# Kernel optimization log

Measured on AMD Instinct MI355X. Metric: run time of the kernel, lower is better.

Reference implementation:

```python
import jax, jax.numpy as jnp
import numpy as np

B, T, W, MODES, NL = 64, 4096, 64, 32, 4
OUT_T = 4096

def _gelu(x):
    # torch.nn.GELU default = exact erf form
    return jax.nn.gelu(x, approximate=False)

def setup_inputs() -> dict:
    key = jax.random.key(0)
    ks = jax.random.split(key, 16)
    scale = 1.0 / (W * W)
    return {
        "x": jax.random.normal(ks[0], (B, T), jnp.float32),
        "lift_w": jax.random.normal(ks[1], (W, 1), jnp.float32) * (1.0 / np.sqrt(1.0)),
        "lift_b": jax.random.normal(ks[2], (W,), jnp.float32) * 0.02,
        "spec_wr": jax.random.normal(ks[3], (NL, W, W, MODES), jnp.float32) * scale,
        "spec_wi": jax.random.normal(ks[4], (NL, W, W, MODES), jnp.float32) * scale,
        "pw_w": jax.random.normal(ks[5], (NL, W, W), jnp.float32) * (1.0 / np.sqrt(W)),
        "pw_b": jax.random.normal(ks[6], (NL, W), jnp.float32) * 0.02,
        "proj1_w": jax.random.normal(ks[7], (W, W), jnp.float32) * (1.0 / np.sqrt(W)),
        "proj1_b": jax.random.normal(ks[8], (W,), jnp.float32) * 0.02,
        "proj2_w": jax.random.normal(ks[9], (1, W), jnp.float32) * (1.0 / np.sqrt(W)),
        "proj2_b": jax.random.normal(ks[10], (1,), jnp.float32) * 0.02,
        "tok_w": jax.random.normal(ks[11], (OUT_T, T), jnp.float32) * (1.0 / np.sqrt(T)),
        "tok_b": jax.random.normal(ks[12], (OUT_T,), jnp.float32) * 0.02,
    }

def reference(x, lift_w, lift_b, spec_wr, spec_wi, pw_w, pw_b,
              proj1_w, proj1_b, proj2_w, proj2_b, tok_w, tok_b):
    # lift: [B,T,1] @ [1,W] -> [B,T,W] -> permute to [B,W,T]
    h = (x[..., None] * lift_w[:, 0][None, None, :] + lift_b)  # [B,T,W]
    h = jnp.transpose(h, (0, 2, 1))  # [B,W,T]
    n_freq = T // 2 + 1
    for l in range(NL):
        xf = jnp.fft.rfft(h, axis=-1)  # [B,W,n_freq] complex64
        w = spec_wr[l] + 1j * spec_wi[l]  # [W,W,MODES]
        out_m = jnp.einsum('bim,iom->bom', xf[:, :, :MODES], w)
        out_ft = jnp.pad(out_m, ((0, 0), (0, 0), (0, n_freq - MODES)))
        spec = jnp.fft.irfft(out_ft, n=T, axis=-1)  # [B,W,T] float32
        pw = jnp.einsum('oi,bit->bot', pw_w[l], h) + pw_b[l][None, :, None]
        h = _gelu(spec + pw)
    h = jnp.transpose(h, (0, 2, 1))  # [B,T,W]
    h = _gelu(h @ proj1_w.T + proj1_b)
    h = (h @ proj2_w.T + proj2_b)[..., 0]  # [B,T]
    return h @ tok_w.T + tok_b  # [B,OUT_T]
```

## Files before the change

kernel.cpp:

```cpp
#include <hip/hip_runtime.h>
#include <math.h>
#include <stdint.h>

#define BB 64
#define TT 4096
#define WW 64
#define MODES 32
#define NLAYER 4
#define OUTT 4096
#define KSPLIT 8
#define KSPLIT_L 16

typedef uint32_t u32;
typedef __attribute__((ext_vector_type(8))) short bf16x8;
typedef __attribute__((ext_vector_type(16))) float f32x16;

#define OFF_HC   0
#define OFF_FTH  16777216
#define OFF_FTL  16908288
#define OFF_ITH  17039360
#define OFF_ITL  17170432
#define OFF_PWH  17301504
#define OFF_PWL  17309696
#define OFF_P1H  17317888
#define OFF_P1L  17319936
#define OFF_YH   17321984
#define OFF_YL   17453056
#define OFF_XFP  17584128
#define OFF_XFB  21778432
#define OFF_SC   22040576
#define OFF_PWLW 22302720
#define OFF_PWLB 22302784
#define OFF_XFXP 22302848
#define OFF_XFXT 22335616

__device__ __forceinline__ float gelu_exact(float x) {
    float ax = fabsf(x);
    float z  = ax * 0.70710678118654752f;
    float t  = __builtin_amdgcn_rcpf(fmaf(0.3275911f, z, 1.0f));
    float ex = __builtin_amdgcn_exp2f(z * z * -1.44269504088896341f);
    float p  = fmaf(fmaf(fmaf(fmaf(1.061405429f, t, -1.453152027f),
                              t, 1.421413741f), t, -0.284496736f), t, 0.254829592f);
    float er = 1.0f - p * t * ex;
    er = copysignf(er, x);
    return 0.5f * x * (1.0f + er);
}
__device__ __forceinline__ u32 bfrn(float f) {
    u32 u = __float_as_uint(f);
    return (u + 0x7fffu + ((u >> 16) & 1u)) >> 16;
}
__device__ __forceinline__ u32 packf(float f) {
    u32 h = bfrn(f);
    float r = f - __uint_as_float(h << 16);
    u32 l = bfrn(r);
    return h | (l << 16);
}
__device__ __forceinline__ void unpack8(const u32* w, bf16x8& hi, bf16x8& lo) {
    union { bf16x8 v; ushort u[8]; } H, L;
    #pragma unroll
    for (int i = 0; i < 8; ++i) { H.u[i] = (ushort)(w[i] & 0xffffu); L.u[i] = (ushort)(w[i] >> 16); }
    hi = H.v; lo = L.v;
}
__device__ __forceinline__ void cvt8(const float* f, bf16x8& hi, bf16x8& lo) {
    union { bf16x8 v; ushort u[8]; } H, L;
    #pragma unroll
    for (int i = 0; i < 8; ++i) {
        u32 h = bfrn(f[i]);
        H.u[i] = (ushort)h;
        L.u[i] = (ushort)bfrn(f[i] - __uint_as_float(h << 16));
    }
    hi = H.v; lo = L.v;
}

#define MM3(ah, al, bh, bl, acc)                                          \
    acc = __builtin_amdgcn_mfma_f32_32x32x16_bf16(ah, bh, acc, 0, 0, 0);  \
    acc = __builtin_amdgcn_mfma_f32_32x32x16_bf16(ah, bl, acc, 0, 0, 0);  \
    acc = __builtin_amdgcn_mfma_f32_32x32x16_bf16(al, bh, acc, 0, 0, 0);

#define ACC_ZERO(acc) { _Pragma("unroll") for (int _i = 0; _i < 16; ++_i) acc[_i] = 0.0f; }

__global__ __launch_bounds__(256) void build_tables_kernel(ushort* __restrict__ fth, ushort* __restrict__ ftl,
                                                           ushort* __restrict__ ith, ushort* __restrict__ itl) {
    const int idx = blockIdx.x * 256 + threadIdx.x;
    const float w0 = 6.28318530717958647692f / (float)TT;
    {
        int pos = idx & 7, l = (idx >> 3) & 63, half = (idx >> 9) & 1, ttile = idx >> 10;
        int j = half * 32 + (l & 31);
        int t = ttile * 16 + (l >> 5) * 8 + pos;
        int m = j & 31;
        float ang = (float)((m * t) & (TT - 1)) * w0;
        float s, c; sincosf(ang, &s, &c);
        u32 p = packf((j < 32) ? c : -s);
        fth[idx] = (ushort)(p & 0xffffu); ftl[idx] = (ushort)(p >> 16);
    }
    {
        int pos = idx & 7, l = (idx >> 3) & 63, kt = (idx >> 9) & 3, t32 = idx >> 11;
        int t = t32 * 32 + (l & 31);
        int j = kt * 16 + (l >> 5) * 8 + pos;
        int m = j & 31;
        float ang = (float)((m * t) & (TT - 1)) * w0;
        float s, c; sincosf(ang, &s, &c);
        float v;
        if (j == 0)       v = 1.0f / (float)TT;
        else if (j < 32)  v = (2.0f / (float)TT) * c;
        else if (j == 32) v = 0.0f;
        else              v = -(2.0f / (float)TT) * s;
        u32 p = packf(v);
        ith[idx] = (ushort)(p & 0xffffu); itl[idx] = (ushort)(p >> 16);
    }
}

__global__ __launch_bounds__(256) void wconv_kernel(const float* __restrict__ pww, const float* __restrict__ p1w,
                                                    const float* __restrict__ lw, const float* __restrict__ lb,
                                                    const float* __restrict__ pwb,
                                                    ushort* __restrict__ pwh, ushort* __restrict__ pwl,
                                                    ushort* __restrict__ p1h, ushort* __restrict__ p1l,
                                                    float* __restrict__ pwlw, float* __restrict__ pwlb) {
    int idx = blockIdx.x * 256 + threadIdx.x;
    if (idx < NLAYER * 4096) {
        int pos = idx & 7, l = (idx >> 3) & 63, kt = (idx >> 9) & 3, half = (idx >> 11) & 1, layer = idx >> 12;
        int o = half * 32 + (l & 31);
        int w = kt * 16 + (l >> 5) * 8 + pos;
        u32 p = packf(pww[layer * 4096 + o * 64 + w]);
        pwh[idx] = (ushort)(p & 0xffffu); pwl[idx] = (ushort)(p >> 16);
    } else if (idx < NLAYER * 4096 + 4096) {
        int k = idx - NLAYER * 4096;
        int pos = k & 7, l = (k >> 3) & 63, kt = (k >> 9) & 3, half = (k >> 11) & 1;
        int wp = half * 32 + (l & 31);
        int w = kt * 16 + (l >> 5) * 8 + pos;
        u32 p = packf(p1w[wp * 64 + w]);
        p1h[k] = (ushort)(p & 0xffffu); p1l[k] = (ushort)(p >> 16);
    } else if (idx < NLAYER * 4096 + 4096 + 64) {
        int o = idx - (NLAYER * 4096 + 4096);
        float aw = 0.f, ab = 0.f;
        for (int w = 0; w < 64; ++w) {
            float pv = pww[o * 64 + w];
            aw += pv * lw[w];
            ab += pv * lb[w];
        }
        pwlw[o] = aw;
        pwlb[o] = ab + pwb[o];
    }
}

__device__ __forceinline__ size_t yfm_idx(int b, int o, int j) {
    return ((((size_t)b * 2 + (o >> 5)) * 4 + (j >> 4)) * 64 + (o & 31) + 32 * ((j >> 3) & 1)) * 8 + (j & 7);
}

__global__ __launch_bounds__(256) void dftx_kernel(const float* __restrict__ x,
                                                   const ushort* __restrict__ fth,
                                                   const ushort* __restrict__ ftl,
                                                   float* __restrict__ xfxp) {
    const int kc = blockIdx.x;
    const int tid = threadIdx.x, l = tid & 63, q = tid >> 6;
    const int mt = q >> 1, nt = q & 1;
    const int bc = nt * 32 + (l & 31);
    const int kh = (l >> 5) * 8;
    f32x16 acc; ACC_ZERO(acc);
    for (int ks = 0; ks < 32; ++ks) {
        int k0 = kc * 512 + ks * 16 + kh;
        size_t fo = (((size_t)(kc * 32 + ks) * 2 + mt) * 64 + l) * 8;
        bf16x8 ah = *(const bf16x8*)(fth + fo);
        bf16x8 al = *(const bf16x8*)(ftl + fo);
        float fbuf[8];
        *(float4*)(fbuf)     = *(const float4*)(x + (size_t)bc * TT + k0);
        *(float4*)(fbuf + 4) = *(const float4*)(x + (size_t)bc * TT + k0 + 4);
        bf16x8 bh, bl; cvt8(fbuf, bh, bl);
        MM3(ah, al, bh, bl, acc);
    }
    #pragma unroll
    for (int r = 0; r < 16; ++r) {
        int j = mt * 32 + (r & 3) + 8 * (r >> 2) + 4 * (l >> 5);
        xfxp[(size_t)kc * 4096 + j * 64 + bc] = acc[r];
    }
}

__global__ __launch_bounds__(256) void xfx_reduce_kernel(const float* __restrict__ xfxp,
                                                         float* __restrict__ xfxT) {
    int idx = blockIdx.x * 256 + threadIdx.x;
    float v = 0.f;
    #pragma unroll
    for (int kc = 0; kc < KSPLIT; ++kc) v += xfxp[(size_t)kc * 4096 + idx];
    xfxT[idx] = v;
}

__global__ __launch_bounds__(256) void specmix0_kernel(const float* __restrict__ xfxT,
                                                       const float* __restrict__ lw,
                                                       const float* __restrict__ lb,
                                                       const float* __restrict__ wr,
                                                       const float* __restrict__ wi,
                                                       ushort* __restrict__ yh,
                                                       ushort* __restrict__ yl) {
    int tid = blockIdx.x * 256 + threadIdx.x;
    int m = tid & 31, o = (tid >> 5) & 63, b = tid >> 11;
    float xvr = xfxT[m * 64 + b];
    float xvi = xfxT[(32 + m) * 64 + b];
    float c0 = (m == 0) ? (float)TT : 0.0f;
    float yr = 0.f, yim = 0.f;
    #pragma unroll 4
    for (int i = 0; i < WW; ++i) {
        float xr = lw[i] * xvr + c0 * lb[i];
        float xi = lw[i] * xvi;
        float ar = wr[((size_t)(i * 64 + o)) * 32 + m];
        float ai = wi[((size_t)(i * 64 + o)) * 32 + m];
        yr  += xr * ar - xi * ai;
        yim += xr * ai + xi * ar;
    }
    u32 pr = packf(yr), pi = packf(yim);
    size_t i0 = yfm_idx(b, o, m), i1 = yfm_idx(b, o, 32 + m);
    yh[i0] = (ushort)(pr & 0xffffu); yl[i0] = (ushort)(pr >> 16);
    yh[i1] = (ushort)(pi & 0xffffu); yl[i1] = (ushort)(pi >> 16);
}

__global__ __launch_bounds__(256) void specmix_kernel(const float* __restrict__ xfb,
                                                      const float* __restrict__ wr,
                                                      const float* __restrict__ wi,
                                                      ushort* __restrict__ yh,
                                                      ushort* __restrict__ yl) {
    int tid = blockIdx.x * 256 + threadIdx.x;
    int m = tid & 31, o = (tid >> 5) & 63, b = tid >> 11;
    float yr = 0.f, yim = 0.f;
    #pragma unroll 4
    for (int i = 0; i < WW; ++i) {
        float xr = xfb[((size_t)(b * 64 + m)) * 64 + i];
        float xi = xfb[((size_t)(b * 64 + 32 + m)) * 64 + i];
        float ar = wr[((size_t)(i * 64 + o)) * 32 + m];
        float ai = wi[((size_t)(i * 64 + o)) * 32 + m];
        yr  += xr * ar - xi * ai;
        yim += xr * ai + xi * ar;
    }
    u32 pr = packf(yr), pi = packf(yim);
    size_t i0 = yfm_idx(b, o, m), i1 = yfm_idx(b, o, 32 + m);
    yh[i0] = (ushort)(pr & 0xffffu); yl[i0] = (ushort)(pr >> 16);
    yh[i1] = (ushort)(pi & 0xffffu); yl[i1] = (ushort)(pi >> 16);
}

__global__ __launch_bounds__(256) void xreduce_kernel(const float* __restrict__ xfp,
                                                      float* __restrict__ xfb) {
    int idx = blockIdx.x * 256 + threadIdx.x;
    float v = 0.f;
    #pragma unroll
    for (int kc = 0; kc < KSPLIT_L; ++kc) v += xfp[(size_t)kc * 262144 + idx];
    xfb[idx] = v;
}

template<int IS_L0>
__global__ __launch_bounds__(256) void layer_kernel(u32* __restrict__ hc,
                                                    const ushort* __restrict__ yh, const ushort* __restrict__ yl,
                                                    const ushort* __restrict__ ith, const ushort* __restrict__ itl,
                                                    const ushort* __restrict__ pwh, const ushort* __restrict__ pwl,
                                                    const float* __restrict__ pwb,
                                                    const float* __restrict__ x,
                                                    const float* __restrict__ pwlw, const float* __restrict__ pwlb,
                                                    const ushort* __restrict__ fth, const ushort* __restrict__ ftl,
                                                    float* __restrict__ xfp) {
    __shared__ u32 lht[2][64 * 68];
    const int kc = blockIdx.x, b = blockIdx.y;
    const int tid = threadIdx.x, l = tid & 63, q = tid >> 6;
    const int mt = q >> 1, nt = q & 1;
    const int ltc = nt * 32 + (l & 31);
    const int kh = (l >> 5) * 8;
    f32x16 aF; ACC_ZERO(aF);

    u32 pf[32];
    if (!IS_L0) {
        const int t32g0 = (kc * 256 >> 5) + nt;
        #pragma unroll
        for (int ks = 0; ks < 4; ++ks) {
            const u32* p = hc + (((size_t)b * 128 + t32g0) * 4 + ks) * 512 + l * 8;
            *(uint4*)(pf + ks * 8)     = *(const uint4*)(p);
            *(uint4*)(pf + ks * 8 + 4) = *(const uint4*)(p + 4);
        }
    }

    for (int tile = 0; tile < 4; ++tile) {
        const int tbase = kc * 256 + tile * 64;
        const int t32g = (tbase >> 5) + nt;
        u32* lbuf = lht[tile & 1];
        f32x16 acc; ACC_ZERO(acc);
        #pragma unroll
        for (int ks = 0; ks < 4; ++ks) {
            size_t yo = (((size_t)b * 2 + mt) * 4 + ks) * 512 + l * 8;
            size_t io = ((size_t)t32g * 4 + ks) * 512 + l * 8;
            bf16x8 ya = *(const bf16x8*)(yh + yo);
            bf16x8 yb = *(const bf16x8*)(yl + yo);
            bf16x8 bh = *(const bf16x8*)(ith + io);
            bf16x8 bl = *(const bf16x8*)(itl + io);
            MM3(ya, yb, bh, bl, acc);
        }
        float xv = 0.f;
        if (!IS_L0) {
            #pragma unroll
            for (int ks = 0; ks < 4; ++ks) {
                size_t po = ((size_t)mt * 4 + ks) * 512 + l * 8;
                bf16x8 pa = *(const bf16x8*)(pwh + po);
                bf16x8 pb = *(const bf16x8*)(pwl + po);
                bf16x8 bh, bl; unpack8(pf + ks * 8, bh, bl);
                MM3(pa, pb, bh, bl, acc);
            }
            if (tile < 3) {
                const int t32n = t32g + 2;
                #pragma unroll
                for (int ks = 0; ks < 4; ++ks) {
                    const u32* p = hc + (((size_t)b * 128 + t32n) * 4 + ks) * 512 + l * 8;
                    *(uint4*)(pf + ks * 8)     = *(const uint4*)(p);
                    *(uint4*)(pf + ks * 8 + 4) = *(const uint4*)(p + 4);
                }
            }
        } else {
            xv = x[(size_t)b * TT + tbase + ltc];
        }
        u32 ov[16];
        #pragma unroll
        for (int rq = 0; rq < 4; ++rq) {
            int ob = mt * 32 + 8 * rq + 4 * (l >> 5);
            #pragma unroll
            for (int i = 0; i < 4; ++i) {
                float v = acc[rq * 4 + i];
                if (IS_L0) v += pwlw[ob + i] * xv + pwlb[ob + i];
                else       v += pwb[ob + i];
                ov[rq * 4 + i] = packf(gelu_exact(v));
            }
        }
        #pragma unroll
        for (int rq = 0; rq < 4; ++rq) {
            int ob = mt * 32 + 8 * rq + 4 * (l >> 5);
            #pragma unroll
            for (int i = 0; i < 4; ++i) lbuf[(ob + i) * 68 + ltc] = ov[rq * 4 + i];
        }
        __syncthreads();
        #pragma unroll
        for (int rq = 0; rq < 4; ++rq) {
            size_t ho = (((size_t)b * 128 + t32g) * 4 + (mt * 2 + (rq >> 1))) * 512
                      + ((l & 31) + 32 * (rq & 1)) * 8 + 4 * (l >> 5);
            *(uint4*)(hc + ho) = *(uint4*)(ov + rq * 4);
        }
        #pragma unroll
        for (int ks = 0; ks < 4; ++ks) {
            int k0 = ks * 16 + kh;
            size_t fo = (((size_t)((tbase >> 4) + ks)) * 2 + mt) * 512 + l * 8;
            bf16x8 ah = *(const bf16x8*)(fth + fo);
            bf16x8 al = *(const bf16x8*)(ftl + fo);
            u32 wbuf[8];
            *(uint4*)(wbuf)     = *(const uint4*)&lbuf[ltc * 68 + k0];
            *(uint4*)(wbuf + 4) = *(const uint4*)&lbuf[ltc * 68 + k0 + 4];
            bf16x8 bh, bl; unpack8(wbuf, bh, bl);
            MM3(ah, al, bh, bl, aF);
        }
    }
    float* dst = xfp + ((size_t)(kc * 64 + b)) * 4096;
    #pragma unroll
    for (int r = 0; r < 16; ++r) {
        int j = mt * 32 + (r & 3) + 8 * (r >> 2) + 4 * (l >> 5);
        dst[j * 64 + ltc] = aF[r];
    }
}

__global__ __launch_bounds__(256) void layer3_kernel(const u32* __restrict__ hc,
                                                     const ushort* __restrict__ yh, const ushort* __restrict__ yl,
                                                     const ushort* __restrict__ ith, const ushort* __restrict__ itl,
                                                     const ushort* __restrict__ pwh, const ushort* __restrict__ pwl,
                                                     const float* __restrict__ pwb,
                                                     const ushort* __restrict__ p1h, const ushort* __restrict__ p1l,
                                                     const float* __restrict__ p1b,
                                                     const float* __restrict__ p2w, const float* __restrict__ p2b,
                                                     u32* __restrict__ sc) {
    __shared__ u32 lht[64 * 68];
    __shared__ float red[4][64];
    const int t0 = blockIdx.x << 6, b = blockIdx.y;
    const int tid = threadIdx.x, l = tid & 63, q = tid >> 6;
    const int mt = q >> 1, nt = q & 1;
    const int ltc = nt * 32 + (l & 31);
    const int kh = (l >> 5) * 8;
    const int t32g = (t0 >> 5) + nt;
    f32x16 acc; ACC_ZERO(acc);

    #pragma unroll
    for (int ks = 0; ks < 4; ++ks) {
        size_t yo = (((size_t)b * 2 + mt) * 4 + ks) * 512 + l * 8;
        size_t io = ((size_t)t32g * 4 + ks) * 512 + l * 8;
        bf16x8 ah = *(const bf16x8*)(yh + yo);
        bf16x8 al = *(const bf16x8*)(yl + yo);
        bf16x8 bh = *(const bf16x8*)(ith + io);
        bf16x8 bl = *(const bf16x8*)(itl + io);
        MM3(ah, al, bh, bl, acc);
    }
    #pragma unroll
    for (int ks = 0; ks < 4; ++ks) {
        size_t po = ((size_t)mt * 4 + ks) * 512 + l * 8;
        bf16x8 ah = *(const bf16x8*)(pwh + po);
        bf16x8 al = *(const bf16x8*)(pwl + po);
        const u32* p = hc + (((size_t)b * 128 + t32g) * 4 + ks) * 512 + l * 8;
        u32 wbuf[8];
        *(uint4*)(wbuf)     = *(const uint4*)(p);
        *(uint4*)(wbuf + 4) = *(const uint4*)(p + 4);
        bf16x8 bh, bl; unpack8(wbuf, bh, bl);
        MM3(ah, al, bh, bl, acc);
    }
    #pragma unroll
    for (int rq = 0; rq < 4; ++rq) {
        int ob = mt * 32 + 8 * rq + 4 * (l >> 5);
        #pragma unroll
        for (int i = 0; i < 4; ++i) {
            float v = acc[rq * 4 + i] + pwb[ob + i];
            lht[(ob + i) * 68 + ltc] = packf(gelu_exact(v));
        }
    }
    __syncthreads();
    f32x16 a2; ACC_ZERO(a2);
    #pragma unroll
    for (int ks = 0; ks < 4; ++ks) {
        int k0 = ks * 16 + kh;
        size_t po = ((size_t)mt * 4 + ks) * 512 + l * 8;
        bf16x8 ah = *(const bf16x8*)(p1h + po);
        bf16x8 al = *(const bf16x8*)(p1l + po);
        u32 wbuf[8];
        #pragma unroll
        for (int i = 0; i < 8; ++i) wbuf[i] = lht[(k0 + i) * 68 + ltc];
        bf16x8 bh, bl; unpack8(wbuf, bh, bl);
        MM3(ah, al, bh, bl, a2);
    }
    float part = 0.f;
    #pragma unroll
    for (int r = 0; r < 16; ++r) {
        int wp = mt * 32 + (r & 3) + 8 * (r >> 2) + 4 * (l >> 5);
        part += gelu_exact(a2[r] + p1b[wp]) * p2w[wp];
    }
    red[q][l] = part;
    __syncthreads();
    if (tid < 64) {
        int hn = tid >> 5, c = tid & 31;
        float v = red[hn][c] + red[hn][c + 32] + red[2 + hn][c] + red[2 + hn][c + 32] + p2b[0];
        int t = t0 + tid;
        size_t so = ((((size_t)(t >> 4)) * 2 + (b >> 5)) * 64 + (b & 31) + 32 * ((t >> 3) & 1)) * 8 + (t & 7);
        sc[so] = packf(v);
    }
}

__global__ __launch_bounds__(256) void tok_kernel(const u32* __restrict__ sc,
                                                  const float* __restrict__ tokw,
                                                  float* __restrict__ tkp) {
    const int u0 = blockIdx.x << 6, kc = blockIdx.y;
    const int tid = threadIdx.x, l = tid & 63, q = tid >> 6;
    const int mt = q >> 1, nt = q & 1;
    const int lu  = u0 + nt * 32 + (l & 31);
    const int kh = (l >> 5) * 8;
    f32x16 acc; ACC_ZERO(acc);
    for (int ks = 0; ks < 32; ++ks) {
        int k0 = kc * 512 + ks * 16 + kh;
        const u32* p = sc + (((size_t)(kc * 32 + ks) * 2 + mt) * 64 + l) * 8;
        u32 wbuf[8];
        *(uint4*)(wbuf)     = *(const uint4*)(p);
        *(uint4*)(wbuf + 4) = *(const uint4*)(p + 4);
        bf16x8 ah, al; unpack8(wbuf, ah, al);
        float fbuf[8];
        const float* tp = tokw + (size_t)lu * TT + k0;
        *(float4*)(fbuf)     = *(const float4*)(tp);
        *(float4*)(fbuf + 4) = *(const float4*)(tp + 4);
        bf16x8 bh, bl; cvt8(fbuf, bh, bl);
        MM3(ah, al, bh, bl, acc);
    }
    #pragma unroll
    for (int r = 0; r < 16; ++r) {
        int br = mt * 32 + (r & 3) + 8 * (r >> 2) + 4 * (l >> 5);
        tkp[((size_t)(kc * 64 + br)) * OUTT + lu] = acc[r];
    }
}

__global__ __launch_bounds__(256) void tok_reduce_kernel(const float* __restrict__ tkp,
                                                         const float* __restrict__ tokb,
                                                         float* __restrict__ out) {
    int idx = blockIdx.x * 256 + threadIdx.x;
    int u = idx & (OUTT - 1);
    float v = tokb[u];
    #pragma unroll
    for (int kc = 0; kc < KSPLIT; ++kc) v += tkp[(size_t)kc * 262144 + idx];
    out[idx] = v;
}

extern "C" void kernel_launch(void* const* d_in, const int* in_sizes, int n_in,
                              void* d_out, int out_size, void* d_ws, size_t ws_size,
                              hipStream_t stream) {
    const float* x    = (const float*)d_in[0];
    const float* lw   = (const float*)d_in[1];
    const float* lb   = (const float*)d_in[2];
    const float* swr  = (const float*)d_in[3];
    const float* swi  = (const float*)d_in[4];
    const float* pww  = (const float*)d_in[5];
    const float* pwb  = (const float*)d_in[6];
    const float* p1w  = (const float*)d_in[7];
    const float* p1b  = (const float*)d_in[8];
    const float* p2w  = (const float*)d_in[9];
    const float* p2b  = (const float*)d_in[10];
    const float* tokw = (const float*)d_in[11];
    const float* tokb = (const float*)d_in[12];
    float* out = (float*)d_out;

    float* ws = (float*)d_ws;
    u32*    hc   = (u32*)(ws + OFF_HC);
    ushort* fth  = (ushort*)(ws + OFF_FTH);
    ushort* ftl  = (ushort*)(ws + OFF_FTL);
    ushort* ith  = (ushort*)(ws + OFF_ITH);
    ushort* itl  = (ushort*)(ws + OFF_ITL);
    ushort* pwh  = (ushort*)(ws + OFF_PWH);
    ushort* pwl  = (ushort*)(ws + OFF_PWL);
    ushort* p1h  = (ushort*)(ws + OFF_P1H);
    ushort* p1l  = (ushort*)(ws + OFF_P1L);
    ushort* yh   = (ushort*)(ws + OFF_YH);
    ushort* yl   = (ushort*)(ws + OFF_YL);
    float*  xfp  = ws + OFF_XFP;
    float*  xfb  = ws + OFF_XFB;
    u32*    sc   = (u32*)(ws + OFF_SC);
    float*  pwlw = ws + OFF_PWLW;
    float*  pwlb = ws + OFF_PWLB;
    float*  xfxp = ws + OFF_XFXP;
    float*  xfxT = ws + OFF_XFXT;

    build_tables_kernel<<<1024, 256, 0, stream>>>(fth, ftl, ith, itl);
    wconv_kernel<<<81, 256, 0, stream>>>(pww, p1w, lw, lb, pwb, pwh, pwl, p1h, p1l, pwlw, pwlb);

    dftx_kernel<<<KSPLIT, 256, 0, stream>>>(x, fth, ftl, xfxp);
    xfx_reduce_kernel<<<16, 256, 0, stream>>>(xfxp, xfxT);
    specmix0_kernel<<<512, 256, 0, stream>>>(xfxT, lw, lb, swr, swi, yh, yl);

    layer_kernel<1><<<dim3(KSPLIT_L, BB), 256, 0, stream>>>(
        hc, yh, yl, ith, itl, pwh, pwl, pwb, x, pwlw, pwlb, fth, ftl, xfp);

    for (int l = 1; l < NLAYER; ++l) {
        xreduce_kernel<<<1024, 256, 0, stream>>>(xfp, xfb);
        specmix_kernel<<<512, 256, 0, stream>>>(
            xfb, swr + (size_t)l * WW * WW * MODES, swi + (size_t)l * WW * WW * MODES, yh, yl);
        if (l < NLAYER - 1) {
            layer_kernel<0><<<dim3(KSPLIT_L, BB), 256, 0, stream>>>(
                hc, yh, yl, ith, itl, pwh + (size_t)l * 4096, pwl + (size_t)l * 4096,
                pwb + (size_t)l * 64, x, pwlw, pwlb, fth, ftl, xfp);
        } else {
            layer3_kernel<<<dim3(TT / 64, BB), 256, 0, stream>>>(
                hc, yh, yl, ith, itl, pwh + (size_t)l * 4096, pwl + (size_t)l * 4096,
                pwb + (size_t)l * 64, p1h, p1l, p1b, p2w, p2b, sc);
        }
    }

    tok_kernel<<<dim3(OUTT / 64, KSPLIT), 256, 0, stream>>>(sc, tokw, xfp);
    tok_reduce_kernel<<<1024, 256, 0, stream>>>(xfp, tokb, out);
}
```

Measured before the change: 272.4 us.

## Split MFMA accumulators, use sincos LUT for tables, raise token GEMM K-split

Splits each three-MFMA chain in the layer kernels across two accumulators so consecutive MFMAs no longer depend on the same accumulator, which shortens the dependency stall between them. Replaces per-element sincosf in the table builder with a 4096-entry cos/sin lookup table computed once by a new small kernel. Raises the K-split of the final token GEMM from 8 to 16 to launch more blocks, at the cost of more partial sums for the reduce kernel to read. The LUT shares workspace with xfxp, and the partial-sum buffer must now hold 16 slices.

```diff
diff --git a/kernel.cpp b/kernel.cpp
--- a/kernel.cpp
+++ b/kernel.cpp
@@ -7,9 +7,10 @@
 #define WW 64
 #define MODES 32
 #define NLAYER 4
+#define KSPLIT 8
+#define KSPLIT_TOK 16
+#define KSPLIT_L 16
 #define OUTT 4096
-#define KSPLIT 8
-#define KSPLIT_L 16
 
 typedef uint32_t u32;
 typedef __attribute__((ext_vector_type(8))) short bf16x8;
@@ -77,19 +78,36 @@
     acc = __builtin_amdgcn_mfma_f32_32x32x16_bf16(ah, bl, acc, 0, 0, 0);  \
     acc = __builtin_amdgcn_mfma_f32_32x32x16_bf16(al, bh, acc, 0, 0, 0);
 
+#define MM3_EVEN(ah, al, bh, bl, accA, accB)                                \
+    accA = __builtin_amdgcn_mfma_f32_32x32x16_bf16(ah, bh, accA, 0, 0, 0);  \
+    accB = __builtin_amdgcn_mfma_f32_32x32x16_bf16(ah, bl, accB, 0, 0, 0);  \
+    accA = __builtin_amdgcn_mfma_f32_32x32x16_bf16(al, bh, accA, 0, 0, 0);
+#define MM3_ODD(ah, al, bh, bl, accA, accB)                                 \
+    accB = __builtin_amdgcn_mfma_f32_32x32x16_bf16(ah, bh, accB, 0, 0, 0);  \
+    accA = __builtin_amdgcn_mfma_f32_32x32x16_bf16(ah, bl, accA, 0, 0, 0);  \
+    accB = __builtin_amdgcn_mfma_f32_32x32x16_bf16(al, bh, accB, 0, 0, 0);
+
 #define ACC_ZERO(acc) { _Pragma("unroll") for (int _i = 0; _i < 16; ++_i) acc[_i] = 0.0f; }
 
-__global__ __launch_bounds__(256) void build_tables_kernel(ushort* __restrict__ fth, ushort* __restrict__ ftl,
+__global__ __launch_bounds__(256) void sincos_lut_kernel(float* __restrict__ lut) {
+    int a = blockIdx.x * 256 + threadIdx.x;
+    const float w0 = 6.28318530717958647692f / (float)TT;
+    float s, c; sincosf((float)a * w0, &s, &c);
+    lut[a * 2]     = c;
+    lut[a * 2 + 1] = s;
+}
+
+__global__ __launch_bounds__(256) void build_tables_kernel(const float* __restrict__ lut,
+                                                           ushort* __restrict__ fth, ushort* __restrict__ ftl,
                                                            ushort* __restrict__ ith, ushort* __restrict__ itl) {
     const int idx = blockIdx.x * 256 + threadIdx.x;
-    const float w0 = 6.28318530717958647692f / (float)TT;
     {
         int pos = idx & 7, l = (idx >> 3) & 63, half = (idx >> 9) & 1, ttile = idx >> 10;
         int j = half * 32 + (l & 31);
         int t = ttile * 16 + (l >> 5) * 8 + pos;
         int m = j & 31;
-        float ang = (float)((m * t) & (TT - 1)) * w0;
-        float s, c; sincosf(ang, &s, &c);
+        int a = (m * t) & (TT - 1);
+        float c = lut[a * 2], s = lut[a * 2 + 1];
         u32 p = packf((j < 32) ? c : -s);
         fth[idx] = (ushort)(p & 0xffffu); ftl[idx] = (ushort)(p >> 16);
     }
@@ -98,8 +116,8 @@
         int t = t32 * 32 + (l & 31);
         int j = kt * 16 + (l >> 5) * 8 + pos;
         int m = j & 31;
-        float ang = (float)((m * t) & (TT - 1)) * w0;
-        float s, c; sincosf(ang, &s, &c);
+        int a = (m * t) & (TT - 1);
+        float c = lut[a * 2], s = lut[a * 2 + 1];
         float v;
         if (j == 0)       v = 1.0f / (float)TT;
         else if (j < 32)  v = (2.0f / (float)TT) * c;
@@ -277,7 +295,7 @@
         const int tbase = kc * 256 + tile * 64;
         const int t32g = (tbase >> 5) + nt;
         u32* lbuf = lht[tile & 1];
-        f32x16 acc; ACC_ZERO(acc);
+        f32x16 accA, accB; ACC_ZERO(accA); ACC_ZERO(accB);
         #pragma unroll
         for (int ks = 0; ks < 4; ++ks) {
             size_t yo = (((size_t)b * 2 + mt) * 4 + ks) * 512 + l * 8;
@@ -286,7 +304,8 @@
             bf16x8 yb = *(const bf16x8*)(yl + yo);
             bf16x8 bh = *(const bf16x8*)(ith + io);
             bf16x8 bl = *(const bf16x8*)(itl + io);
-            MM3(ya, yb, bh, bl, acc);
+            if (ks & 1) { MM3_ODD(ya, yb, bh, bl, accA, accB); }
+            else        { MM3_EVEN(ya, yb, bh, bl, accA, accB); }
         }
         float xv = 0.f;
         if (!IS_L0) {
@@ -296,7 +315,8 @@
                 bf16x8 pa = *(const bf16x8*)(pwh + po);
                 bf16x8 pb = *(const bf16x8*)(pwl + po);
                 bf16x8 bh, bl; unpack8(pf + ks * 8, bh, bl);
-                MM3(pa, pb, bh, bl, acc);
+                if (ks & 1) { MM3_ODD(pa, pb, bh, bl, accA, accB); }
+                else        { MM3_EVEN(pa, pb, bh, bl, accA, accB); }
             }
             if (tile < 3) {
                 const int t32n = t32g + 2;
@@ -316,7 +336,7 @@
             int ob = mt * 32 + 8 * rq + 4 * (l >> 5);
             #pragma unroll
             for (int i = 0; i < 4; ++i) {
-                float v = acc[rq * 4 + i];
+                float v = accA[rq * 4 + i] + accB[rq * 4 + i];
                 if (IS_L0) v += pwlw[ob + i] * xv + pwlb[ob + i];
                 else       v += pwb[ob + i];
                 ov[rq * 4 + i] = packf(gelu_exact(v));
@@ -373,7 +393,7 @@
     const int ltc = nt * 32 + (l & 31);
     const int kh = (l >> 5) * 8;
     const int t32g = (t0 >> 5) + nt;
-    f32x16 acc; ACC_ZERO(acc);
+    f32x16 accA, accB; ACC_ZERO(accA); ACC_ZERO(accB);
 
     #pragma unroll
     for (int ks = 0; ks < 4; ++ks) {
@@ -383,7 +403,8 @@
         bf16x8 al = *(const bf16x8*)(yl + yo);
         bf16x8 bh = *(const bf16x8*)(ith + io);
         bf16x8 bl = *(const bf16x8*)(itl + io);
-        MM3(ah, al, bh, bl, acc);
+        if (ks & 1) { MM3_ODD(ah, al, bh, bl, accA, accB); }
+        else        { MM3_EVEN(ah, al, bh, bl, accA, accB); }
     }
     #pragma unroll
     for (int ks = 0; ks < 4; ++ks) {
@@ -395,14 +416,15 @@
         *(uint4*)(wbuf)     = *(const uint4*)(p);
         *(uint4*)(wbuf + 4) = *(const uint4*)(p + 4);
         bf16x8 bh, bl; unpack8(wbuf, bh, bl);
-        MM3(ah, al, bh, bl, acc);
+        if (ks & 1) { MM3_ODD(ah, al, bh, bl, accA, accB); }
+        else        { MM3_EVEN(ah, al, bh, bl, accA, accB); }
     }
     #pragma unroll
     for (int rq = 0; rq < 4; ++rq) {
         int ob = mt * 32 + 8 * rq + 4 * (l >> 5);
         #pragma unroll
         for (int i = 0; i < 4; ++i) {
-            float v = acc[rq * 4 + i] + pwb[ob + i];
+            float v = accA[rq * 4 + i] + accB[rq * 4 + i] + pwb[ob + i];
             lht[(ob + i) * 68 + ltc] = packf(gelu_exact(v));
         }
     }
@@ -446,9 +468,9 @@
     const int lu  = u0 + nt * 32 + (l & 31);
     const int kh = (l >> 5) * 8;
     f32x16 acc; ACC_ZERO(acc);
-    for (int ks = 0; ks < 32; ++ks) {
-        int k0 = kc * 512 + ks * 16 + kh;
-        const u32* p = sc + (((size_t)(kc * 32 + ks) * 2 + mt) * 64 + l) * 8;
+    for (int ks = 0; ks < 4096 / KSPLIT_TOK / 16; ++ks) {
+        int k0 = kc * (4096 / KSPLIT_TOK) + ks * 16 + kh;
+        const u32* p = sc + (((size_t)((kc * (4096 / KSPLIT_TOK) / 16) + ks) * 2 + mt) * 64 + l) * 8;
         u32 wbuf[8];
         *(uint4*)(wbuf)     = *(const uint4*)(p);
         *(uint4*)(wbuf + 4) = *(const uint4*)(p + 4);
@@ -474,7 +496,7 @@
     int u = idx & (OUTT - 1);
     float v = tokb[u];
     #pragma unroll
-    for (int kc = 0; kc < KSPLIT; ++kc) v += tkp[(size_t)kc * 262144 + idx];
+    for (int kc = 0; kc < KSPLIT_TOK; ++kc) v += tkp[(size_t)kc * 262144 + idx];
     out[idx] = v;
 }
 
@@ -515,8 +537,10 @@
     float*  pwlb = ws + OFF_PWLB;
     float*  xfxp = ws + OFF_XFXP;
     float*  xfxT = ws + OFF_XFXT;
-
-    build_tables_kernel<<<1024, 256, 0, stream>>>(fth, ftl, ith, itl);
+    float*  lut  = ws + OFF_XFXP;
+
+    sincos_lut_kernel<<<16, 256, 0, stream>>>(lut);
+    build_tables_kernel<<<1024, 256, 0, stream>>>(lut, fth, ftl, ith, itl);
     wconv_kernel<<<81, 256, 0, stream>>>(pww, p1w, lw, lb, pwb, pwh, pwl, p1h, p1l, pwlw, pwlb);
 
     dftx_kernel<<<KSPLIT, 256, 0, stream>>>(x, fth, ftl, xfxp);
@@ -541,6 +565,6 @@
         }
     }
 
-    tok_kernel<<<dim3(OUTT / 64, KSPLIT), 256, 0, stream>>>(sc, tokw, xfp);
+    tok_kernel<<<dim3(OUTT / 64, KSPLIT_TOK), 256, 0, stream>>>(sc, tokw, xfp);
     tok_reduce_kernel<<<1024, 256, 0, stream>>>(xfp, tokb, out);
 }
```

Result: no change. 270.3 us (-0.8%).
